# Kernel tuning notes

Hardware: AMD Instinct MI355X
Metric: run time of the kernel (lower is better)

Reference implementation:

```python
import jax, jax.numpy as jnp
import numpy as np

IN, H, C = 128, 512, 32
B, T = 64, 512


def _gru_cell(x, h, W_ih, W_hh, b_ih, b_hh):
    # PyTorch GRUCell: gates ordered (r, z, n)
    gi = x @ W_ih.T + b_ih          # [B, 3H]
    gh = h @ W_hh.T + b_hh          # [B, 3H]
    i_r, i_z, i_n = jnp.split(gi, 3, axis=-1)
    h_r, h_z, h_n = jnp.split(gh, 3, axis=-1)
    r = jax.nn.sigmoid(i_r + h_r)
    z = jax.nn.sigmoid(i_z + h_z)
    n = jnp.tanh(i_n + r * h_n)
    return (1.0 - z) * n + z * h


def setup_inputs() -> dict:
    key = jax.random.key(0)
    ks = jax.random.split(key, 20)
    d = {
        "x": jax.random.normal(ks[0], (B, T, IN), dtype=jnp.float32),
        "h0_1": 0.1 * jax.random.normal(ks[1], (B, H), dtype=jnp.float32),
        "h0_2": 0.1 * jax.random.normal(ks[2], (B, H), dtype=jnp.float32),
        "h0_3": 0.1 * jax.random.normal(ks[3], (B, H), dtype=jnp.float32),
    }
    ins = [IN, H, H]
    i = 4
    for l in range(3):
        s_in = 1.0 / np.sqrt(ins[l])
        d[f"W_ih{l+1}"] = s_in * jax.random.normal(ks[i], (3 * H, ins[l]), dtype=jnp.float32); i += 1
        d[f"W_hh{l+1}"] = (1.0 / np.sqrt(H)) * jax.random.normal(ks[i], (3 * H, H), dtype=jnp.float32); i += 1
        d[f"b_ih{l+1}"] = jnp.zeros((3 * H,), dtype=jnp.float32)
        d[f"b_hh{l+1}"] = jnp.zeros((3 * H,), dtype=jnp.float32)
    d["W_out"] = (1.0 / np.sqrt(H)) * jax.random.normal(ks[i], (C, H), dtype=jnp.float32); i += 1
    d["b_out"] = jax.random.uniform(ks[i], (C,), dtype=jnp.float32)
    return d


def reference(x, h0_1, h0_2, h0_3,
              W_ih1, W_hh1, b_ih1, b_hh1,
              W_ih2, W_hh2, b_ih2, b_hh2,
              W_ih3, W_hh3, b_ih3, b_hh3,
              W_out, b_out):
    xT = jnp.transpose(x, (1, 0, 2))  # [T, B, IN]

    def step(carry, xt):
        h1, h2, h3 = carry
        h1 = _gru_cell(xt, h1, W_ih1, W_hh1, b_ih1, b_hh1)
        h2 = _gru_cell(h1, h2, W_ih2, W_hh2, b_ih2, b_hh2)
        h3 = _gru_cell(h2, h3, W_ih3, W_hh3, b_ih3, b_hh3)
        y = jax.nn.softmax(h3 @ W_out.T + b_out, axis=1)  # [B, C]
        return (h1, h2, h3), y

    _, Y = jax.lax.scan(step, (h0_1, h0_2, h0_3), xT)  # Y: [T, B, C]
    return jnp.transpose(Y, (1, 0, 2))  # [B, T, C]
```

## Files before the change

### kernel.cpp

```cpp
#include <hip/hip_runtime.h>

typedef unsigned short u16;
typedef unsigned int u32;
typedef unsigned long long u64;
typedef __attribute__((ext_vector_type(8))) short bf16x8;
typedef __attribute__((ext_vector_type(4))) float f32x4;

#define T_ 512
#define B_ 64
#define IN_ 128
#define H_ 512
#define C_ 32
#define BH_ (B_ * H_)
#define NWG_LAYER 64
#define NWG_CELL 192
#define NWG_TOT 196
#define NGRP 7
#define NT 515

#define DEVINL __device__ __attribute__((always_inline)) inline

DEVINL u16 f2bf_(float f) {
    u32 u = __float_as_uint(f);
    u32 r = (u + 0x7FFFu + ((u >> 16) & 1u)) >> 16;
    return (u16)r;
}
DEVINL float bf2f_(u16 h) { return __uint_as_float(((u32)h) << 16); }

DEVINL u64 ld_llc_u64(const u64* p) {
    return __hip_atomic_load((u64*)p, __ATOMIC_RELAXED, __HIP_MEMORY_SCOPE_AGENT);
}
DEVINL void st_llc_u32(u32* p, u32 v) {
    __hip_atomic_store(p, v, __ATOMIC_RELAXED, __HIP_MEMORY_SCOPE_AGENT);
}

__global__ void split_kernel(const float* __restrict__ src, u16* __restrict__ hi,
                             u16* __restrict__ lo, int n) {
    int i = blockIdx.x * 256 + threadIdx.x;
    if (i < n) {
        float f = src[i];
        u16 h = f2bf_(f);
        hi[i] = h;
        lo[i] = f2bf_(f - bf2f_(h));
    }
}

struct Params {
    const float* x;
    const u16* ih_hi[3]; const u16* ih_lo[3];
    const u16* hh_hi[3]; const u16* hh_lo[3];
    const float* b_ih[3]; const float* b_hh[3];
    const u16* wout_hi; const u16* wout_lo;
    const float* b_out;
    u16* h_hi; u16* h_lo;
    u32* bar;
    float* y;
};

DEVINL void grid_barrier(u32* bar, int wg, int tid, u32 tick) {
    __syncthreads();
    if (tid == 0) {
        const int g = wg >> 5;
        const u32 gsz = (g == NGRP - 1) ? (u32)(NWG_TOT - 32 * (NGRP - 1)) : 32u;
        u32 old = __hip_atomic_fetch_add(&bar[g * 32], 1u,
                                         __ATOMIC_RELAXED, __HIP_MEMORY_SCOPE_AGENT);
        if (old == (tick + 1u) * gsz - 1u) {
            u32 o2 = __hip_atomic_fetch_add(&bar[NGRP * 32], 1u,
                                            __ATOMIC_RELAXED, __HIP_MEMORY_SCOPE_AGENT);
            if (o2 == (tick + 1u) * (u32)NGRP - 1u)
                __hip_atomic_store(&bar[NGRP * 32 + 32], tick + 1u,
                                   __ATOMIC_RELAXED, __HIP_MEMORY_SCOPE_AGENT);
        }
        while (__hip_atomic_load(&bar[NGRP * 32 + 32],
                                 __ATOMIC_RELAXED, __HIP_MEMORY_SCOPE_AGENT) < tick + 1u) {
            __builtin_amdgcn_s_sleep(1);
        }
    }
    __syncthreads();
}

DEVINL bf16x8 ld8(const u16* p) { return *reinterpret_cast<const bf16x8*>(p); }

DEVINL bf16x8 ld8_lds(const u16* s, int row, int kb) {
    const int bo = (row << 10) + (((kb) << 1) ^ ((row & 7) << 4));
    return *reinterpret_cast<const bf16x8*>((const char*)s + bo);
}

DEVINL f32x4 mfma3(bf16x8 ah, bf16x8 al, bf16x8 bh, bf16x8 bl, f32x4 c) {
    c = __builtin_amdgcn_mfma_f32_16x16x32_bf16(ah, bh, c, 0, 0, 0);
    c = __builtin_amdgcn_mfma_f32_16x16x32_bf16(al, bh, c, 0, 0, 0);
    c = __builtin_amdgcn_mfma_f32_16x16x32_bf16(ah, bl, c, 0, 0, 0);
    return c;
}

DEVINL void gemm3_reg(const u16* sAh, const u16* sAl, int row,
                      const bf16x8 (&w)[3][2][16], int lhi,
                      f32x4& o0, f32x4& o1, f32x4& o2) {
    f32x4 a0 = {0.f,0.f,0.f,0.f}, a1 = {0.f,0.f,0.f,0.f}, a2 = {0.f,0.f,0.f,0.f};
#pragma unroll
    for (int kt = 0; kt < 16; ++kt) {
        const int kb = kt * 32 + lhi * 8;
        bf16x8 ah = ld8_lds(sAh, row, kb), al = ld8_lds(sAl, row, kb);
        a0 = mfma3(ah, al, w[0][0][kt], w[0][1][kt], a0);
        a1 = mfma3(ah, al, w[1][0][kt], w[1][1][kt], a1);
        a2 = mfma3(ah, al, w[2][0][kt], w[2][1][kt], a2);
    }
    o0 = a0; o1 = a1; o2 = a2;
}

DEVINL void gemm2_reg(const u16* sAh, const u16* sAl, int row,
                      const bf16x8 (&w)[3][2][16], int lhi,
                      f32x4& o0, f32x4& o1) {
    f32x4 a0 = {0.f,0.f,0.f,0.f}, a1 = {0.f,0.f,0.f,0.f};
#pragma unroll
    for (int kt = 0; kt < 16; ++kt) {
        const int kb = kt * 32 + lhi * 8;
        bf16x8 ah = ld8_lds(sAh, row, kb), al = ld8_lds(sAl, row, kb);
        a0 = mfma3(ah, al, w[0][0][kt], w[0][1][kt], a0);
        a1 = mfma3(ah, al, w[1][0][kt], w[1][1][kt], a1);
    }
    o0 = a0; o1 = a1;
}

DEVINL void stage_h(const u16* ghi, const u16* glo,
                    u16* shi, u16* slo, int b0, int tid) {
#pragma unroll
    for (int c = 0; c < 2; ++c) {
        u64 rh[4], rl[4];
#pragma unroll
        for (int k = 0; k < 4; ++k) {
            const int idx = tid + ((c * 4 + k) << 8);
            const int row = idx >> 7, col = idx & 127;
            rh[k] = ld_llc_u64((const u64*)(ghi + (size_t)(b0 + row) * H_) + col);
            rl[k] = ld_llc_u64((const u64*)(glo + (size_t)(b0 + row) * H_) + col);
        }
#pragma unroll
        for (int k = 0; k < 4; ++k) {
            const int idx = tid + ((c * 4 + k) << 8);
            const int row = idx >> 7;
            const int so = (row << 10) + (((idx & 127) << 3) ^ ((row & 7) << 4));
            *(u64*)((char*)shi + so) = rh[k];
            *(u64*)((char*)slo + so) = rl[k];
        }
    }
}

DEVINL void store_sg(float (&dst)[16][33], f32x4 a, int col, int lhi) {
#pragma unroll
    for (int q = 0; q < 4; ++q) dst[lhi * 4 + q][col] = a[q];
}

__global__ __launch_bounds__(256, 1) void gru_pipe(Params p) {
    __shared__ u16 hs[4][8192];
    __shared__ float sg[6][16][33];
    __shared__ float slog[16][33];
    const int wg = blockIdx.x, tid = threadIdx.x;
    const int wave = tid >> 6, lane = tid & 63;
    const int ln15 = lane & 15, lhi = lane >> 4;

    bf16x8 wreg[3][2][16];
    const int L = (wg < NWG_CELL) ? (wg >> 6) : 0;
    const int wgl = wg & 63, ug = wgl & 15, mb = wgl >> 4;
    const int u0 = ug * 32, b0c = mb * 16;
    const int tt0 = wave * 3;
    if (wg < NWG_CELL) {
        if (wave >= 2) {
#pragma unroll
            for (int j = 0; j < 3; ++j) {
                const int tt = tt0 + j, g = (tt >> 1) - 3, c = (tt & 1) * 16 + ln15;
                const u16* bh = p.hh_hi[L] + (size_t)(g * H_ + u0 + c) * H_;
                const u16* bl = p.hh_lo[L] + (size_t)(g * H_ + u0 + c) * H_;
#pragma unroll
                for (int kt = 0; kt < 16; ++kt) {
                    wreg[j][0][kt] = ld8(bh + kt * 32 + lhi * 8);
                    wreg[j][1][kt] = ld8(bl + kt * 32 + lhi * 8);
                }
            }
        } else if (L > 0) {
#pragma unroll
            for (int j = 0; j < 3; ++j) {
                const int tt = tt0 + j, g = tt >> 1, c = (tt & 1) * 16 + ln15;
                const u16* bh = p.ih_hi[L] + (size_t)(g * H_ + u0 + c) * H_;
                const u16* bl = p.ih_lo[L] + (size_t)(g * H_ + u0 + c) * H_;
#pragma unroll
                for (int kt = 0; kt < 16; ++kt) {
                    wreg[j][0][kt] = ld8(bh + kt * 32 + lhi * 8);
                    wreg[j][1][kt] = ld8(bl + kt * 32 + lhi * 8);
                }
            }
        } else {
#pragma unroll
            for (int j = 0; j < 3; ++j) {
                const int tt = tt0 + j, g = tt >> 1, c = (tt & 1) * 16 + ln15;
                const u16* bh = p.ih_hi[0] + (size_t)(g * H_ + u0 + c) * IN_;
                const u16* bl = p.ih_lo[0] + (size_t)(g * H_ + u0 + c) * IN_;
#pragma unroll
                for (int kt = 0; kt < 4; ++kt) {
                    wreg[j][0][kt] = ld8(bh + kt * 32 + lhi * 8);
                    wreg[j][1][kt] = ld8(bl + kt * 32 + lhi * 8);
                }
            }
        }
    } else if (wave == 0) {
#pragma unroll
        for (int j = 0; j < 2; ++j) {
            const u16* bh = p.wout_hi + (size_t)(j * 16 + ln15) * H_;
            const u16* bl = p.wout_lo + (size_t)(j * 16 + ln15) * H_;
#pragma unroll
            for (int kt = 0; kt < 16; ++kt) {
                wreg[j][0][kt] = ld8(bh + kt * 32 + lhi * 8);
                wreg[j][1][kt] = ld8(bl + kt * 32 + lhi * 8);
            }
        }
    }

    for (int u = 0; u < NT; ++u) {
        if (wg < NWG_CELL) {
            const int t = u - L;
            if (t >= 0 && t < T_) {
                const int rs = t & 1, wsl = rs ^ 1;
                const u16* hp_hi = p.h_hi + (size_t)(2 * L + rs) * BH_;
                const u16* hp_lo = p.h_lo + (size_t)(2 * L + rs) * BH_;
                stage_h(hp_hi, hp_lo, hs[0], hs[1], b0c, tid);
                if (L > 0) {
                    const u16* hi_hi = p.h_hi + (size_t)(2 * (L - 1) + wsl) * BH_;
                    const u16* hi_lo = p.h_lo + (size_t)(2 * (L - 1) + wsl) * BH_;
                    stage_h(hi_hi, hi_lo, hs[2], hs[3], b0c, tid);
                }
                __syncthreads();

                f32x4 oA, oB, oC;
                if (wave < 2 && L == 0) {
                    const float* xr = p.x + (size_t)(b0c + ln15) * (T_ * IN_) + (size_t)t * IN_;
                    f32x4 a0 = {0.f,0.f,0.f,0.f}, a1 = {0.f,0.f,0.f,0.f}, a2 = {0.f,0.f,0.f,0.f};
#pragma unroll
                    for (int kt = 0; kt < 4; ++kt) {
                        const int kb = kt * 32 + lhi * 8;
                        bf16x8 ah, al;
#pragma unroll
                        for (int j = 0; j < 8; ++j) {
                            float f = xr[kb + j];
                            u16 hb = f2bf_(f);
                            ah[j] = (short)hb;
                            al[j] = (short)f2bf_(f - bf2f_(hb));
                        }
                        a0 = mfma3(ah, al, wreg[0][0][kt], wreg[0][1][kt], a0);
                        a1 = mfma3(ah, al, wreg[1][0][kt], wreg[1][1][kt], a1);
                        a2 = mfma3(ah, al, wreg[2][0][kt], wreg[2][1][kt], a2);
                    }
                    oA = a0; oB = a1; oC = a2;
                } else {
                    const u16* sAh = (wave < 2) ? hs[2] : hs[0];
                    const u16* sAl = (wave < 2) ? hs[3] : hs[1];
                    gemm3_reg(sAh, sAl, ln15, wreg, lhi, oA, oB, oC);
                }
                {
                    const int gA = (tt0    ) >> 1, cA = ((tt0    ) & 1) * 16 + ln15;
                    const int gB = (tt0 + 1) >> 1, cB = ((tt0 + 1) & 1) * 16 + ln15;
                    const int gC = (tt0 + 2) >> 1, cC = ((tt0 + 2) & 1) * 16 + ln15;
                    store_sg(sg[gA], oA, cA, lhi);
                    store_sg(sg[gB], oB, cB, lhi);
                    store_sg(sg[gC], oC, cC, lhi);
                }
                __syncthreads();

                {
                    const int rb = tid & 15, uu = tid >> 4;
                    const int colu = uu * 2;
                    const int gcol = u0 + colu;
                    const int bo = (colu * 2 + ((u0 & 511) * 2)) ^ ((rb & 7) << 4);
                    const u32 hp2h = *(const u32*)((const char*)hs[0] + (rb << 10) + ((gcol * 2) ^ ((rb & 7) << 4)));
                    const u32 hp2l = *(const u32*)((const char*)hs[1] + (rb << 10) + ((gcol * 2) ^ ((rb & 7) << 4)));
                    (void)bo;
                    u32 packh = 0, packl = 0;
#pragma unroll
                    for (int half = 0; half < 2; ++half) {
                        const int uc = colu + half;
                        const int uidx = u0 + uc;
                        const float ir  = sg[0][rb][uc] + p.b_ih[L][uidx];
                        const float iz  = sg[1][rb][uc] + p.b_ih[L][H_ + uidx];
                        const float in_ = sg[2][rb][uc] + p.b_ih[L][2 * H_ + uidx];
                        const float hr  = sg[3][rb][uc] + p.b_hh[L][uidx];
                        const float hz  = sg[4][rb][uc] + p.b_hh[L][H_ + uidx];
                        const float hn  = sg[5][rb][uc] + p.b_hh[L][2 * H_ + uidx];
                        const float r = 1.f / (1.f + expf(-(ir + hr)));
                        const float z = 1.f / (1.f + expf(-(iz + hz)));
                        const float n = tanhf(in_ + r * hn);
                        const float hprev = bf2f_((u16)((half ? (hp2h >> 16) : hp2h) & 0xffffu))
                                          + bf2f_((u16)((half ? (hp2l >> 16) : hp2l) & 0xffffu));
                        const float hnew = (1.f - z) * n + z * hprev;
                        const u16 nh = f2bf_(hnew);
                        const u16 nl = f2bf_(hnew - bf2f_(nh));
                        packh |= (u32)nh << (16 * half);
                        packl |= (u32)nl << (16 * half);
                    }
                    u16* ho_hi = p.h_hi + (size_t)(2 * L + wsl) * BH_;
                    u16* ho_lo = p.h_lo + (size_t)(2 * L + wsl) * BH_;
                    const size_t hx = (size_t)(b0c + rb) * H_ + gcol;
                    st_llc_u32((u32*)(ho_hi + hx), packh);
                    st_llc_u32((u32*)(ho_lo + hx), packl);
                }
            }
        } else {
            const int t = u - 3;
            if (t >= 0) {
                const int slot = (t + 1) & 1;
                const int b0 = (wg - NWG_CELL) * 16;
                const u16* Ah = p.h_hi + (size_t)(4 + slot) * BH_;
                const u16* Al = p.h_lo + (size_t)(4 + slot) * BH_;
                stage_h(Ah, Al, hs[0], hs[1], b0, tid);
                __syncthreads();
                if (wave == 0) {
                    f32x4 a0, a1;
                    gemm2_reg(hs[0], hs[1], ln15, wreg, lhi, a0, a1);
#pragma unroll
                    for (int q = 0; q < 4; ++q) {
                        slog[lhi * 4 + q][ln15] = a0[q];
                        slog[lhi * 4 + q][16 + ln15] = a1[q];
                    }
                }
                __syncthreads();
                if (tid < 16) {
                    float v[32];
                    float m = -1e30f;
#pragma unroll
                    for (int c = 0; c < 32; ++c) { v[c] = slog[tid][c] + p.b_out[c]; m = fmaxf(m, v[c]); }
                    float s = 0.f;
#pragma unroll
                    for (int c = 0; c < 32; ++c) { v[c] = expf(v[c] - m); s += v[c]; }
                    const float inv = 1.f / s;
                    float* yp = p.y + ((size_t)(b0 + tid) * T_ + t) * C_;
#pragma unroll
                    for (int c = 0; c < 32; ++c) yp[c] = v[c] * inv;
                }
            }
        }
        grid_barrier(p.bar, wg, tid, (u32)u);
    }
}

extern "C" void kernel_launch(void* const* d_in, const int* in_sizes, int n_in,
                              void* d_out, int out_size, void* d_ws, size_t ws_size,
                              hipStream_t stream) {
    (void)in_sizes; (void)n_in; (void)out_size; (void)ws_size;

    const float* x      = (const float*)d_in[0];
    const float* h0[3]  = {(const float*)d_in[1], (const float*)d_in[2], (const float*)d_in[3]};
    const float* Wih[3] = {(const float*)d_in[4], (const float*)d_in[8], (const float*)d_in[12]};
    const float* Whh[3] = {(const float*)d_in[5], (const float*)d_in[9], (const float*)d_in[13]};
    const float* bih[3] = {(const float*)d_in[6], (const float*)d_in[10], (const float*)d_in[14]};
    const float* bhh[3] = {(const float*)d_in[7], (const float*)d_in[11], (const float*)d_in[15]};
    const float* Wout   = (const float*)d_in[16];
    const float* bout   = (const float*)d_in[17];

    u16* w = (u16*)d_ws;
    size_t off = 0;
    auto take = [&](size_t n) { u16* p = w + off; off += n; return p; };
    u16 *ihh[3], *ihl[3], *hhh[3], *hhl[3];
    const size_t szih[3] = {(size_t)3 * H_ * IN_, (size_t)3 * H_ * H_, (size_t)3 * H_ * H_};
    const size_t szhh = (size_t)3 * H_ * H_;
    for (int l = 0; l < 3; ++l) {
        ihh[l] = take(szih[l]); ihl[l] = take(szih[l]);
        hhh[l] = take(szhh);    hhl[l] = take(szhh);
    }
    u16* wouth = take((size_t)C_ * H_);
    u16* woutl = take((size_t)C_ * H_);
    u16* hhi = take((size_t)3 * 2 * BH_);
    u16* hlo = take((size_t)3 * 2 * BH_);
    off = (off + 255) & ~(size_t)255;
    u32* bar = (u32*)take(2 * ((NGRP + 2) * 32));
    const size_t bar_bytes = (size_t)(NGRP + 2) * 32 * sizeof(u32);

    hipMemsetAsync(bar, 0, bar_bytes, stream);

    auto split = [&](const float* src, u16* hi, u16* lo, int n) {
        split_kernel<<<dim3((n + 255) / 256), dim3(256), 0, stream>>>(src, hi, lo, n);
    };
    for (int l = 0; l < 3; ++l) {
        split(Wih[l], ihh[l], ihl[l], (int)szih[l]);
        split(Whh[l], hhh[l], hhl[l], (int)szhh);
    }
    split(Wout, wouth, woutl, C_ * H_);
    for (int l = 0; l < 3; ++l)
        split(h0[l], hhi + (size_t)(2 * l) * BH_, hlo + (size_t)(2 * l) * BH_, BH_);

    Params p;
    p.x = x;
    for (int l = 0; l < 3; ++l) {
        p.ih_hi[l] = ihh[l]; p.ih_lo[l] = ihl[l];
        p.hh_hi[l] = hhh[l]; p.hh_lo[l] = hhl[l];
        p.b_ih[l] = bih[l];  p.b_hh[l] = bhh[l];
    }
    p.wout_hi = wouth; p.wout_lo = woutl; p.b_out = bout;
    p.h_hi = hhi; p.h_lo = hlo;
    p.bar = bar;
    p.y = (float*)d_out;

    void* args[] = {&p};
    hipError_t err = hipLaunchCooperativeKernel((void*)gru_pipe, dim3(NWG_TOT), dim3(256),
                                                args, 0u, stream);
    if (err != hipSuccess) {
        gru_pipe<<<dim3(NWG_TOT), dim3(256), 0, stream>>>(p);
    }
}
```

Measured before the change: 3.424 ms.

## Replace global grid barrier with per-layer per-batch-block dataflow flags

Removes the global grid barrier that ran on every pipeline tick and replaces it with fine-grained counters and flags, one set per (layer, batch-block). Each workgroup waits only on the producers it depends on: its own layer's previous step and the previous layer's current step. It also waits on reader-release flags before overwriting a slot. Hidden-state buffers go from double to triple buffering so layers can drift apart by a step. This is meant to cut global synchronisation latency and let independent batch blocks proceed asynchronously, at the cost of more flag traffic and a subtler correctness protocol built on relaxed atomics.

```diff
diff --git a/kernel.cpp b/kernel.cpp
--- a/kernel.cpp
+++ b/kernel.cpp
@@ -12,11 +12,15 @@
 #define H_ 512
 #define C_ 32
 #define BH_ (B_ * H_)
-#define NWG_LAYER 64
 #define NWG_CELL 192
 #define NWG_TOT 196
-#define NGRP 7
-#define NT 515
+
+#define FA(L, mb)       ((((L) * 4 + (mb))) * 32)
+#define FG(L, mb)       (((12 + (L) * 4 + (mb))) * 32)
+#define FRA(Lm, mb, s)  (((24 + ((Lm) * 4 + (mb)) * 3 + (s))) * 32)
+#define FRG(Lm, mb, s)  (((48 + ((Lm) * 4 + (mb)) * 3 + (s))) * 32)
+#define FO(mb, s)       (((72 + (mb) * 3 + (s))) * 32)
+#define NFLAG 84
 
 #define DEVINL __device__ __attribute__((always_inline)) inline
 
@@ -32,6 +36,18 @@
 }
 DEVINL void st_llc_u32(u32* p, u32 v) {
     __hip_atomic_store(p, v, __ATOMIC_RELAXED, __HIP_MEMORY_SCOPE_AGENT);
+}
+DEVINL u32 ld_flag(u32* p) {
+    return __hip_atomic_load(p, __ATOMIC_RELAXED, __HIP_MEMORY_SCOPE_AGENT);
+}
+DEVINL u32 add_flag(u32* p) {
+    return __hip_atomic_fetch_add(p, 1u, __ATOMIC_RELAXED, __HIP_MEMORY_SCOPE_AGENT);
+}
+DEVINL void st_flag(u32* p, u32 v) {
+    __hip_atomic_store(p, v, __ATOMIC_RELAXED, __HIP_MEMORY_SCOPE_AGENT);
+}
+DEVINL void wait_ge(u32* p, u32 v) {
+    while (ld_flag(p) < v) __builtin_amdgcn_s_sleep(1);
 }
 
 __global__ void split_kernel(const float* __restrict__ src, u16* __restrict__ hi,
@@ -57,28 +73,6 @@
     float* y;
 };
 
-DEVINL void grid_barrier(u32* bar, int wg, int tid, u32 tick) {
-    __syncthreads();
-    if (tid == 0) {
-        const int g = wg >> 5;
-        const u32 gsz = (g == NGRP - 1) ? (u32)(NWG_TOT - 32 * (NGRP - 1)) : 32u;
-        u32 old = __hip_atomic_fetch_add(&bar[g * 32], 1u,
-                                         __ATOMIC_RELAXED, __HIP_MEMORY_SCOPE_AGENT);
-        if (old == (tick + 1u) * gsz - 1u) {
-            u32 o2 = __hip_atomic_fetch_add(&bar[NGRP * 32], 1u,
-                                            __ATOMIC_RELAXED, __HIP_MEMORY_SCOPE_AGENT);
-            if (o2 == (tick + 1u) * (u32)NGRP - 1u)
-                __hip_atomic_store(&bar[NGRP * 32 + 32], tick + 1u,
-                                   __ATOMIC_RELAXED, __HIP_MEMORY_SCOPE_AGENT);
-        }
-        while (__hip_atomic_load(&bar[NGRP * 32 + 32],
-                                 __ATOMIC_RELAXED, __HIP_MEMORY_SCOPE_AGENT) < tick + 1u) {
-            __builtin_amdgcn_s_sleep(1);
-        }
-    }
-    __syncthreads();
-}
-
 DEVINL bf16x8 ld8(const u16* p) { return *reinterpret_cast<const bf16x8*>(p); }
 
 DEVINL bf16x8 ld8_lds(const u16* s, int row, int kb) {
@@ -157,12 +151,14 @@
     const int wg = blockIdx.x, tid = threadIdx.x;
     const int wave = tid >> 6, lane = tid & 63;
     const int ln15 = lane & 15, lhi = lane >> 4;
+    u32* F = p.bar;
 
     bf16x8 wreg[3][2][16];
     const int L = (wg < NWG_CELL) ? (wg >> 6) : 0;
     const int wgl = wg & 63, ug = wgl & 15, mb = wgl >> 4;
     const int u0 = ug * 32, b0c = mb * 16;
     const int tt0 = wave * 3;
+    (void)ug;
     if (wg < NWG_CELL) {
         if (wave >= 2) {
 #pragma unroll
@@ -214,128 +210,141 @@
         }
     }
 
-    for (int u = 0; u < NT; ++u) {
-        if (wg < NWG_CELL) {
-            const int t = u - L;
-            if (t >= 0 && t < T_) {
-                const int rs = t & 1, wsl = rs ^ 1;
-                const u16* hp_hi = p.h_hi + (size_t)(2 * L + rs) * BH_;
-                const u16* hp_lo = p.h_lo + (size_t)(2 * L + rs) * BH_;
-                stage_h(hp_hi, hp_lo, hs[0], hs[1], b0c, tid);
-                if (L > 0) {
-                    const u16* hi_hi = p.h_hi + (size_t)(2 * (L - 1) + wsl) * BH_;
-                    const u16* hi_lo = p.h_lo + (size_t)(2 * (L - 1) + wsl) * BH_;
-                    stage_h(hi_hi, hi_lo, hs[2], hs[3], b0c, tid);
-                }
-                __syncthreads();
-
-                f32x4 oA, oB, oC;
-                if (wave < 2 && L == 0) {
-                    const float* xr = p.x + (size_t)(b0c + ln15) * (T_ * IN_) + (size_t)t * IN_;
-                    f32x4 a0 = {0.f,0.f,0.f,0.f}, a1 = {0.f,0.f,0.f,0.f}, a2 = {0.f,0.f,0.f,0.f};
-#pragma unroll
-                    for (int kt = 0; kt < 4; ++kt) {
-                        const int kb = kt * 32 + lhi * 8;
-                        bf16x8 ah, al;
-#pragma unroll
-                        for (int j = 0; j < 8; ++j) {
-                            float f = xr[kb + j];
-                            u16 hb = f2bf_(f);
-                            ah[j] = (short)hb;
-                            al[j] = (short)f2bf_(f - bf2f_(hb));
-                        }
-                        a0 = mfma3(ah, al, wreg[0][0][kt], wreg[0][1][kt], a0);
-                        a1 = mfma3(ah, al, wreg[1][0][kt], wreg[1][1][kt], a1);
-                        a2 = mfma3(ah, al, wreg[2][0][kt], wreg[2][1][kt], a2);
+    if (wg < NWG_CELL) {
+        for (int t = 0; t < T_; ++t) {
+            const int sCur = t % 3, sPrev = (t + 2) % 3;
+            if (tid == 0) {
+                wait_ge(&F[FG(L, mb)], (u32)t);
+                if (L > 0) wait_ge(&F[FG(L - 1, mb)], (u32)(t + 1));
+            }
+            __syncthreads();
+            stage_h(p.h_hi + (size_t)(3 * L + sPrev) * BH_,
+                    p.h_lo + (size_t)(3 * L + sPrev) * BH_, hs[0], hs[1], b0c, tid);
+            if (L > 0)
+                stage_h(p.h_hi + (size_t)(3 * (L - 1) + sCur) * BH_,
+                        p.h_lo + (size_t)(3 * (L - 1) + sCur) * BH_, hs[2], hs[3], b0c, tid);
+            __syncthreads();
+            if (tid == 0 && L > 0) {
+                const u32 k = (u32)(t / 3) + 1u;
+                u32 old = add_flag(&F[FRA(L - 1, mb, sCur)]);
+                if (old == 16u * k - 1u) st_flag(&F[FRG(L - 1, mb, sCur)], k);
+            }
+
+            f32x4 oA, oB, oC;
+            if (wave < 2 && L == 0) {
+                const float* xr = p.x + (size_t)(b0c + ln15) * (T_ * IN_) + (size_t)t * IN_;
+                f32x4 a0 = {0.f,0.f,0.f,0.f}, a1 = {0.f,0.f,0.f,0.f}, a2 = {0.f,0.f,0.f,0.f};
+#pragma unroll
+                for (int kt = 0; kt < 4; ++kt) {
+                    const int kb = kt * 32 + lhi * 8;
+                    bf16x8 ah, al;
+#pragma unroll
+                    for (int j = 0; j < 8; ++j) {
+                        float f = xr[kb + j];
+                        u16 hb = f2bf_(f);
+                        ah[j] = (short)hb;
+                        al[j] = (short)f2bf_(f - bf2f_(hb));
                     }
-                    oA = a0; oB = a1; oC = a2;
-                } else {
-                    const u16* sAh = (wave < 2) ? hs[2] : hs[0];
-                    const u16* sAl = (wave < 2) ? hs[3] : hs[1];
-                    gemm3_reg(sAh, sAl, ln15, wreg, lhi, oA, oB, oC);
-                }
-                {
-                    const int gA = (tt0    ) >> 1, cA = ((tt0    ) & 1) * 16 + ln15;
-                    const int gB = (tt0 + 1) >> 1, cB = ((tt0 + 1) & 1) * 16 + ln15;
-                    const int gC = (tt0 + 2) >> 1, cC = ((tt0 + 2) & 1) * 16 + ln15;
-                    store_sg(sg[gA], oA, cA, lhi);
-                    store_sg(sg[gB], oB, cB, lhi);
-                    store_sg(sg[gC], oC, cC, lhi);
-                }
-                __syncthreads();
-
-                {
-                    const int rb = tid & 15, uu = tid >> 4;
-                    const int colu = uu * 2;
-                    const int gcol = u0 + colu;
-                    const int bo = (colu * 2 + ((u0 & 511) * 2)) ^ ((rb & 7) << 4);
-                    const u32 hp2h = *(const u32*)((const char*)hs[0] + (rb << 10) + ((gcol * 2) ^ ((rb & 7) << 4)));
-                    const u32 hp2l = *(const u32*)((const char*)hs[1] + (rb << 10) + ((gcol * 2) ^ ((rb & 7) << 4)));
-                    (void)bo;
-                    u32 packh = 0, packl = 0;
-#pragma unroll
-                    for (int half = 0; half < 2; ++half) {
-                        const int uc = colu + half;
-                        const int uidx = u0 + uc;
-                        const float ir  = sg[0][rb][uc] + p.b_ih[L][uidx];
-                        const float iz  = sg[1][rb][uc] + p.b_ih[L][H_ + uidx];
-                        const float in_ = sg[2][rb][uc] + p.b_ih[L][2 * H_ + uidx];
-                        const float hr  = sg[3][rb][uc] + p.b_hh[L][uidx];
-                        const float hz  = sg[4][rb][uc] + p.b_hh[L][H_ + uidx];
-                        const float hn  = sg[5][rb][uc] + p.b_hh[L][2 * H_ + uidx];
-                        const float r = 1.f / (1.f + expf(-(ir + hr)));
-                        const float z = 1.f / (1.f + expf(-(iz + hz)));
-                        const float n = tanhf(in_ + r * hn);
-                        const float hprev = bf2f_((u16)((half ? (hp2h >> 16) : hp2h) & 0xffffu))
-                                          + bf2f_((u16)((half ? (hp2l >> 16) : hp2l) & 0xffffu));
-                        const float hnew = (1.f - z) * n + z * hprev;
-                        const u16 nh = f2bf_(hnew);
-                        const u16 nl = f2bf_(hnew - bf2f_(nh));
-                        packh |= (u32)nh << (16 * half);
-                        packl |= (u32)nl << (16 * half);
-                    }
-                    u16* ho_hi = p.h_hi + (size_t)(2 * L + wsl) * BH_;
-                    u16* ho_lo = p.h_lo + (size_t)(2 * L + wsl) * BH_;
-                    const size_t hx = (size_t)(b0c + rb) * H_ + gcol;
-                    st_llc_u32((u32*)(ho_hi + hx), packh);
-                    st_llc_u32((u32*)(ho_lo + hx), packl);
-                }
-            }
-        } else {
-            const int t = u - 3;
-            if (t >= 0) {
-                const int slot = (t + 1) & 1;
-                const int b0 = (wg - NWG_CELL) * 16;
-                const u16* Ah = p.h_hi + (size_t)(4 + slot) * BH_;
-                const u16* Al = p.h_lo + (size_t)(4 + slot) * BH_;
-                stage_h(Ah, Al, hs[0], hs[1], b0, tid);
-                __syncthreads();
-                if (wave == 0) {
-                    f32x4 a0, a1;
-                    gemm2_reg(hs[0], hs[1], ln15, wreg, lhi, a0, a1);
-#pragma unroll
-                    for (int q = 0; q < 4; ++q) {
-                        slog[lhi * 4 + q][ln15] = a0[q];
-                        slog[lhi * 4 + q][16 + ln15] = a1[q];
-                    }
-                }
-                __syncthreads();
-                if (tid < 16) {
-                    float v[32];
-                    float m = -1e30f;
-#pragma unroll
-                    for (int c = 0; c < 32; ++c) { v[c] = slog[tid][c] + p.b_out[c]; m = fmaxf(m, v[c]); }
-                    float s = 0.f;
-#pragma unroll
-                    for (int c = 0; c < 32; ++c) { v[c] = expf(v[c] - m); s += v[c]; }
-                    const float inv = 1.f / s;
-                    float* yp = p.y + ((size_t)(b0 + tid) * T_ + t) * C_;
-#pragma unroll
-                    for (int c = 0; c < 32; ++c) yp[c] = v[c] * inv;
-                }
-            }
-        }
-        grid_barrier(p.bar, wg, tid, (u32)u);
+                    a0 = mfma3(ah, al, wreg[0][0][kt], wreg[0][1][kt], a0);
+                    a1 = mfma3(ah, al, wreg[1][0][kt], wreg[1][1][kt], a1);
+                    a2 = mfma3(ah, al, wreg[2][0][kt], wreg[2][1][kt], a2);
+                }
+                oA = a0; oB = a1; oC = a2;
+            } else {
+                const u16* sAh = (wave < 2) ? hs[2] : hs[0];
+                const u16* sAl = (wave < 2) ? hs[3] : hs[1];
+                gemm3_reg(sAh, sAl, ln15, wreg, lhi, oA, oB, oC);
+            }
+            {
+                const int gA = (tt0    ) >> 1, cA = ((tt0    ) & 1) * 16 + ln15;
+                const int gB = (tt0 + 1) >> 1, cB = ((tt0 + 1) & 1) * 16 + ln15;
+                const int gC = (tt0 + 2) >> 1, cC = ((tt0 + 2) & 1) * 16 + ln15;
+                store_sg(sg[gA], oA, cA, lhi);
+                store_sg(sg[gB], oB, cB, lhi);
+                store_sg(sg[gC], oC, cC, lhi);
+            }
+            __syncthreads();
+            if (tid == 0 && t >= 3) {
+                const u32 k = (u32)((t - 3) / 3) + 1u;
+                if (L < 2) wait_ge(&F[FRG(L, mb, sCur)], k);
+                else       wait_ge(&F[FO(mb, sCur)], k);
+            }
+            __syncthreads();
+
+            {
+                const int rb = tid & 15, uu = tid >> 4;
+                const int colu = uu * 2;
+                const int gcol = u0 + colu;
+                const u32 hp2h = *(const u32*)((const char*)hs[0] + (rb << 10) + ((gcol * 2) ^ ((rb & 7) << 4)));
+                const u32 hp2l = *(const u32*)((const char*)hs[1] + (rb << 10) + ((gcol * 2) ^ ((rb & 7) << 4)));
+                u32 packh = 0, packl = 0;
+#pragma unroll
+                for (int half = 0; half < 2; ++half) {
+                    const int uc = colu + half;
+                    const int uidx = u0 + uc;
+                    const float ir  = sg[0][rb][uc] + p.b_ih[L][uidx];
+                    const float iz  = sg[1][rb][uc] + p.b_ih[L][H_ + uidx];
+                    const float in_ = sg[2][rb][uc] + p.b_ih[L][2 * H_ + uidx];
+                    const float hr  = sg[3][rb][uc] + p.b_hh[L][uidx];
+                    const float hz  = sg[4][rb][uc] + p.b_hh[L][H_ + uidx];
+                    const float hn  = sg[5][rb][uc] + p.b_hh[L][2 * H_ + uidx];
+                    const float r = 1.f / (1.f + expf(-(ir + hr)));
+                    const float z = 1.f / (1.f + expf(-(iz + hz)));
+                    const float n = tanhf(in_ + r * hn);
+                    const float hprev = bf2f_((u16)((half ? (hp2h >> 16) : hp2h) & 0xffffu))
+                                      + bf2f_((u16)((half ? (hp2l >> 16) : hp2l) & 0xffffu));
+                    const float hnew = (1.f - z) * n + z * hprev;
+                    const u16 nh = f2bf_(hnew);
+                    const u16 nl = f2bf_(hnew - bf2f_(nh));
+                    packh |= (u32)nh << (16 * half);
+                    packl |= (u32)nl << (16 * half);
+                }
+                u16* ho_hi = p.h_hi + (size_t)(3 * L + sCur) * BH_;
+                u16* ho_lo = p.h_lo + (size_t)(3 * L + sCur) * BH_;
+                const size_t hx = (size_t)(b0c + rb) * H_ + gcol;
+                st_llc_u32((u32*)(ho_hi + hx), packh);
+                st_llc_u32((u32*)(ho_lo + hx), packl);
+            }
+            __syncthreads();
+            if (tid == 0) {
+                u32 old = add_flag(&F[FA(L, mb)]);
+                if (old == 16u * (u32)(t + 1) - 1u) st_flag(&F[FG(L, mb)], (u32)(t + 1));
+            }
+        }
+    } else {
+        const int mbo = wg - NWG_CELL, b0 = mbo * 16;
+        for (int t = 0; t < T_; ++t) {
+            const int s = t % 3;
+            if (tid == 0) wait_ge(&F[FG(2, mbo)], (u32)(t + 1));
+            __syncthreads();
+            stage_h(p.h_hi + (size_t)(6 + s) * BH_, p.h_lo + (size_t)(6 + s) * BH_,
+                    hs[0], hs[1], b0, tid);
+            __syncthreads();
+            if (tid == 0) add_flag(&F[FO(mbo, s)]);
+            if (wave == 0) {
+                f32x4 a0, a1;
+                gemm2_reg(hs[0], hs[1], ln15, wreg, lhi, a0, a1);
+#pragma unroll
+                for (int q = 0; q < 4; ++q) {
+                    slog[lhi * 4 + q][ln15] = a0[q];
+                    slog[lhi * 4 + q][16 + ln15] = a1[q];
+                }
+            }
+            __syncthreads();
+            if (tid < 16) {
+                float v[32];
+                float m = -1e30f;
+#pragma unroll
+                for (int c = 0; c < 32; ++c) { v[c] = slog[tid][c] + p.b_out[c]; m = fmaxf(m, v[c]); }
+                float sden = 0.f;
+#pragma unroll
+                for (int c = 0; c < 32; ++c) { v[c] = expf(v[c] - m); sden += v[c]; }
+                const float inv = 1.f / sden;
+                float* yp = p.y + ((size_t)(b0 + tid) * T_ + t) * C_;
+#pragma unroll
+                for (int c = 0; c < 32; ++c) yp[c] = v[c] * inv;
+            }
+        }
     }
 }
 
@@ -365,11 +374,11 @@
     }
     u16* wouth = take((size_t)C_ * H_);
     u16* woutl = take((size_t)C_ * H_);
-    u16* hhi = take((size_t)3 * 2 * BH_);
-    u16* hlo = take((size_t)3 * 2 * BH_);
+    u16* hhi = take((size_t)3 * 3 * BH_);
+    u16* hlo = take((size_t)3 * 3 * BH_);
     off = (off + 255) & ~(size_t)255;
-    u32* bar = (u32*)take(2 * ((NGRP + 2) * 32));
-    const size_t bar_bytes = (size_t)(NGRP + 2) * 32 * sizeof(u32);
+    u32* bar = (u32*)take(2 * (NFLAG * 32));
+    const size_t bar_bytes = (size_t)NFLAG * 32 * sizeof(u32);
 
     hipMemsetAsync(bar, 0, bar_bytes, stream);
 
@@ -382,7 +391,7 @@
     }
     split(Wout, wouth, woutl, C_ * H_);
     for (int l = 0; l < 3; ++l)
-        split(h0[l], hhi + (size_t)(2 * l) * BH_, hlo + (size_t)(2 * l) * BH_, BH_);
+        split(h0[l], hhi + (size_t)(3 * l + 2) * BH_, hlo + (size_t)(3 * l + 2) * BH_, BH_);
 
     Params p;
     p.x = x;
```

New measurement: 3.251 ms. 5.1% less time.
